# Kernel tuning notes

Hardware: AMD Instinct MI355X
Metric: run time of the kernel (lower is better)

## Reference

```python
import jax, jax.numpy as jnp
import numpy as np

THRESH = 1.0
DECAY = 0.5


def setup_inputs() -> dict:
    key = jax.random.key(0)
    X = jax.random.normal(key, (64, 128, 32, 32, 8), dtype=jnp.float32)
    return {"X": X}


def reference(X):
    # X: [..., T]; sequential LIF recurrence over the last axis via lax.scan.
    Xt = jnp.moveaxis(X, -1, 0)  # [T, ...]

    def step(mem, x):
        mem = mem * DECAY + x
        s = (mem >= THRESH).astype(X.dtype)  # hard heaviside spike
        mem = mem * (1.0 - s)                # reset fired neurons
        return mem, s

    mem0 = jnp.zeros(Xt.shape[1:], dtype=X.dtype)
    _, spikes = jax.lax.scan(step, mem0, Xt)  # spikes: [T, ...]
    return jnp.moveaxis(spikes, 0, -1)        # [..., T]
```

## Files before the change

### kernel.cpp

```cpp
#include <hip/hip_runtime.h>

#define THRESH 1.0f
#define DECAY  0.5f

typedef float f32x4 __attribute__((ext_vector_type(4)));

constexpr int BLOCK = 256;
constexpr int NEUR_PER_THREAD = 2;
constexpr int TILE_NEURONS = BLOCK * NEUR_PER_THREAD;
constexpr int PAD = 12;

__global__ __launch_bounds__(BLOCK) void lif_kernel(const float* __restrict__ X,
                                                    float* __restrict__ S,
                                                    long long n_neurons) {
    __shared__ float lds[TILE_NEURONS * PAD];
    const int tid = threadIdx.x;
    const long long tile = blockIdx.x;
    const long long base_neuron = tile * TILE_NEURONS;
    const long long base_f4 = base_neuron * 2;
    const long long total_f4 = n_neurons * 2;

    const f32x4* __restrict__ Xv = reinterpret_cast<const f32x4*>(X);
    f32x4* __restrict__ Sv = reinterpret_cast<f32x4*>(S);

#pragma unroll
    for (int r = 0; r < NEUR_PER_THREAD; ++r) {
        int ln = tid + r * BLOCK;
        long long gn = base_neuron + ln;
        if (gn < n_neurons) {
            f32x4 a = Xv[gn * 2];
            f32x4 b = Xv[gn * 2 + 1];
            float xv[8] = {a[0], a[1], a[2], a[3], b[0], b[1], b[2], b[3]};
            float sv[8];
            float mem = 0.0f;
#pragma unroll
            for (int t = 0; t < 8; ++t) {
                mem = mem * DECAY + xv[t];
                bool fired = (mem >= THRESH);
                sv[t] = fired ? 1.0f : 0.0f;
                mem   = fired ? 0.0f : mem;
            }
            *reinterpret_cast<f32x4*>(&lds[ln * PAD + 0]) = (f32x4){sv[0], sv[1], sv[2], sv[3]};
            *reinterpret_cast<f32x4*>(&lds[ln * PAD + 4]) = (f32x4){sv[4], sv[5], sv[6], sv[7]};
        }
    }
    __syncthreads();

#pragma unroll
    for (int k = 0; k < 4; ++k) {
        int g = tid + k * BLOCK;
        long long gi = base_f4 + g;
        if (gi < total_f4) {
            int neuron = g >> 1;
            int e4 = (g & 1) * 4;
            f32x4 s = *reinterpret_cast<const f32x4*>(&lds[neuron * PAD + e4]);
            __builtin_nontemporal_store(s, &Sv[gi]);
        }
    }
}

extern "C" void kernel_launch(void* const* d_in, const int* in_sizes, int n_in,
                              void* d_out, int out_size, void* d_ws, size_t ws_size,
                              hipStream_t stream) {
    const float* X = (const float*)d_in[0];
    float* S = (float*)d_out;
    long long n_elems   = (long long)in_sizes[0];
    long long n_neurons = n_elems / 8;

    long long n_tiles = (n_neurons + TILE_NEURONS - 1) / TILE_NEURONS;
    lif_kernel<<<(int)n_tiles, BLOCK, 0, stream>>>(X, S, n_neurons);
}
```

Baseline: 80.49 us.

## Use persistent grid-stride blocks with register prefetch and double-buffered LDS

Replaces the one-tile-per-block launch with a persistent grid capped at 2048 blocks that loop over tiles. Each block loads the next tile's inputs into registers while it writes out the current tile, and the LDS staging buffer is double-buffered. The aim is to overlap loads with stores and cut block launch overhead in this memory-bound kernel. The cost is lower memory-level parallelism from fewer resident blocks, plus double the LDS per block, which may lower occupancy.

```diff
diff --git a/kernel.cpp b/kernel.cpp
--- a/kernel.cpp
+++ b/kernel.cpp
@@ -6,56 +6,82 @@
 typedef float f32x4 __attribute__((ext_vector_type(4)));
 
 constexpr int BLOCK = 256;
-constexpr int NEUR_PER_THREAD = 2;
-constexpr int TILE_NEURONS = BLOCK * NEUR_PER_THREAD;
+constexpr int NPT = 2;
+constexpr int TILE = BLOCK * NPT;
 constexpr int PAD = 12;
 
 __global__ __launch_bounds__(BLOCK) void lif_kernel(const float* __restrict__ X,
                                                     float* __restrict__ S,
                                                     long long n_neurons) {
-    __shared__ float lds[TILE_NEURONS * PAD];
+    __shared__ float lds[2][TILE * PAD];
     const int tid = threadIdx.x;
-    const long long tile = blockIdx.x;
-    const long long base_neuron = tile * TILE_NEURONS;
-    const long long base_f4 = base_neuron * 2;
+    const long long n_tiles  = (n_neurons + TILE - 1) / TILE;
     const long long total_f4 = n_neurons * 2;
 
     const f32x4* __restrict__ Xv = reinterpret_cast<const f32x4*>(X);
     f32x4* __restrict__ Sv = reinterpret_cast<f32x4*>(S);
 
+    long long tile = blockIdx.x;
+    if (tile >= n_tiles) return;
+
+    f32x4 a[NPT], b[NPT];
 #pragma unroll
-    for (int r = 0; r < NEUR_PER_THREAD; ++r) {
-        int ln = tid + r * BLOCK;
-        long long gn = base_neuron + ln;
-        if (gn < n_neurons) {
-            f32x4 a = Xv[gn * 2];
-            f32x4 b = Xv[gn * 2 + 1];
-            float xv[8] = {a[0], a[1], a[2], a[3], b[0], b[1], b[2], b[3]};
-            float sv[8];
-            float mem = 0.0f;
-#pragma unroll
-            for (int t = 0; t < 8; ++t) {
-                mem = mem * DECAY + xv[t];
-                bool fired = (mem >= THRESH);
-                sv[t] = fired ? 1.0f : 0.0f;
-                mem   = fired ? 0.0f : mem;
-            }
-            *reinterpret_cast<f32x4*>(&lds[ln * PAD + 0]) = (f32x4){sv[0], sv[1], sv[2], sv[3]};
-            *reinterpret_cast<f32x4*>(&lds[ln * PAD + 4]) = (f32x4){sv[4], sv[5], sv[6], sv[7]};
-        }
+    for (int r = 0; r < NPT; ++r) {
+        long long gn = tile * TILE + tid + r * BLOCK;
+        if (gn < n_neurons) { a[r] = Xv[2 * gn]; b[r] = Xv[2 * gn + 1]; }
     }
-    __syncthreads();
+
+    int cur = 0;
+    while (true) {
+        const long long next = tile + gridDim.x;
 
 #pragma unroll
-    for (int k = 0; k < 4; ++k) {
-        int g = tid + k * BLOCK;
-        long long gi = base_f4 + g;
-        if (gi < total_f4) {
-            int neuron = g >> 1;
-            int e4 = (g & 1) * 4;
-            f32x4 s = *reinterpret_cast<const f32x4*>(&lds[neuron * PAD + e4]);
-            __builtin_nontemporal_store(s, &Sv[gi]);
+        for (int r = 0; r < NPT; ++r) {
+            int ln = tid + r * BLOCK;
+            long long gn = tile * TILE + ln;
+            if (gn < n_neurons) {
+                float xv[8] = {a[r][0], a[r][1], a[r][2], a[r][3],
+                               b[r][0], b[r][1], b[r][2], b[r][3]};
+                float sv[8];
+                float mem = 0.0f;
+#pragma unroll
+                for (int t = 0; t < 8; ++t) {
+                    mem = mem * DECAY + xv[t];
+                    bool fired = (mem >= THRESH);
+                    sv[t] = fired ? 1.0f : 0.0f;
+                    mem   = fired ? 0.0f : mem;
+                }
+                *reinterpret_cast<f32x4*>(&lds[cur][ln * PAD + 0]) = (f32x4){sv[0], sv[1], sv[2], sv[3]};
+                *reinterpret_cast<f32x4*>(&lds[cur][ln * PAD + 4]) = (f32x4){sv[4], sv[5], sv[6], sv[7]};
+            }
         }
+
+        if (next < n_tiles) {
+#pragma unroll
+            for (int r = 0; r < NPT; ++r) {
+                long long gn = next * TILE + tid + r * BLOCK;
+                if (gn < n_neurons) { a[r] = Xv[2 * gn]; b[r] = Xv[2 * gn + 1]; }
+            }
+        }
+
+        __syncthreads();
+
+        const long long base_f4 = tile * (long long)TILE * 2;
+#pragma unroll
+        for (int k = 0; k < 4; ++k) {
+            int g = tid + k * BLOCK;
+            long long gi = base_f4 + g;
+            if (gi < total_f4) {
+                int neuron = g >> 1;
+                int e4 = (g & 1) * 4;
+                f32x4 s = *reinterpret_cast<const f32x4*>(&lds[cur][neuron * PAD + e4]);
+                __builtin_nontemporal_store(s, &Sv[gi]);
+            }
+        }
+
+        if (next >= n_tiles) break;
+        tile = next;
+        cur ^= 1;
     }
 }
 
@@ -67,6 +93,7 @@
     long long n_elems   = (long long)in_sizes[0];
     long long n_neurons = n_elems / 8;
 
-    long long n_tiles = (n_neurons + TILE_NEURONS - 1) / TILE_NEURONS;
-    lif_kernel<<<(int)n_tiles, BLOCK, 0, stream>>>(X, S, n_neurons);
+    long long n_tiles = (n_neurons + TILE - 1) / TILE;
+    int grid = (int)(n_tiles < 2048 ? n_tiles : 2048);
+    lif_kernel<<<grid, BLOCK, 0, stream>>>(X, S, n_neurons);
 }
```

Measured after the change: 81.39 us. Within noise of the previous version (+1.1%).
